# Optimization experiments

Hardware: AMD Instinct MI355X
Metric: run time of the kernel (lower is better)

The kernel has to match this reference:

```python
import jax, jax.numpy as jnp
from jax import lax
import numpy as np

BETA, TAU, NUM_ITER = 0.33, 1.0, 5
DN = ('NCDHW', 'OIDHW', 'NCDHW')


def _base_kernels():
    # 3x3x3 neighborhood-counting kernels from the torch module
    K_N6 = np.zeros((3, 3, 3), np.float32)
    for c in [(1, 1, 0), (1, 1, 2), (1, 0, 1), (1, 2, 1), (0, 1, 1), (2, 1, 1)]:
        K_N6[c] = 1.0
    K_N26 = np.ones((3, 3, 3), np.float32); K_N26[1, 1, 1] = 0.0
    K_N18 = K_N26.copy()
    for c in [(0, 0, 0), (0, 0, 2), (0, 2, 0), (0, 2, 2), (2, 0, 0), (2, 0, 2), (2, 2, 0), (2, 2, 2)]:
        K_N18[c] = 0.0
    K_B26 = np.zeros((3, 3, 3), np.float32)
    K_B26[0, 0, 0] = 1.0
    for c in [(0, 0, 1), (0, 1, 0), (0, 1, 1), (1, 0, 0), (1, 0, 1), (1, 1, 0)]:
        K_B26[c] = -1.0
    K_A6 = np.zeros((3, 3, 3), np.float32)
    K_A6[0, 1, 1] = -1.0
    for c in [(0, 0, 1), (0, 1, 0), (0, 1, 2), (0, 2, 1)]:
        K_A6[c] = 1.0
    return K_N6, K_N26, K_N18, K_B26, K_A6


def _stacked_weight():
    # Fuse all 17 simple-check convolutions into one conv over a 3-channel input
    # channel 0: img, channel 1: 1-img, channel 2: 2*img-1
    K_N6, K_N26, K_N18, K_B26, K_A6 = _base_kernels()
    b26 = [K_B26] + [np.flip(K_B26, ax) for ax in [(0,), (1,), (2,), (0, 1), (0, 2), (1, 2), (0, 1, 2)]]
    fA = np.flip(K_A6, 0)
    a6 = [K_A6, np.rot90(K_A6, axes=(0, 1)), np.rot90(K_A6, axes=(0, 2)),
          fA, np.rot90(fA, axes=(0, 1)), np.rot90(fA, axes=(0, 2))]
    rows = []
    def put(k, ch):
        w = np.zeros((3, 3, 3, 3), np.float32)
        w[ch] = k
        rows.append(w)
    put(K_N6, 1)   # counts bg 6-neighbors (applied to 1-img)
    put(K_N26, 0)  # counts fg 26-neighbors
    put(K_N18, 0)  # counts fg 18-neighbors
    for k in b26:
        put(k, 2)  # 8 B26-cell detectors on 2*img-1
    for k in a6:
        put(k, 2)  # 6 A6-cell detectors on 2*img-1
    return jnp.asarray(np.stack(rows)), jnp.asarray(K_N26).reshape(1, 1, 3, 3, 3)


W_SIMPLE, W_N26 = _stacked_weight()


def _clip01(x):  # F.hardtanh(x, 0, 1)
    return jnp.clip(x, 0.0, 1.0)


def _endpoint_check(img):
    p = jnp.pad(img, ((0, 0), (0, 0), (1, 1), (1, 1), (1, 1)))
    n26 = lax.conv_general_dilated(p, W_N26, (1, 1, 1), 'VALID', dimension_numbers=DN)
    return _clip01(2.0 - n26)  # endpoint iff <=1 fg 26-neighbor


def _simple_check(img):
    p = jnp.pad(img, ((0, 0), (0, 0), (1, 1), (1, 1), (1, 1)))
    x3 = jnp.concatenate([p, 1.0 - p, 2.0 * p - 1.0], axis=1)
    f = lax.conv_general_dilated(x3, W_SIMPLE, (2, 2, 2), 'VALID', dimension_numbers=DN)
    n6, n26, n18 = f[:, 0:1], f[:, 1:2], f[:, 2:3]
    num_b26 = jax.nn.relu(f[:, 3:11] - 6.0).sum(axis=1, keepdims=True)
    num_a6 = jax.nn.relu(f[:, 11:17] - 4.0).sum(axis=1, keepdims=True)
    cond1 = _clip01(n6) * _clip01(2.0 - n6)                              # exactly one bg 6-neighbor
    cond2 = _clip01(n26) * _clip01(2.0 - n26)                            # exactly one fg 26-neighbor
    cond3 = _clip01(n18) * _clip01(2.0 - n18) * _clip01(1.0 - num_b26)   # one 18-neighbor, no B26 cell
    cond4 = _clip01(n6 - 1.0) * _clip01(1.0 - num_a6) * _clip01(1.0 - num_b26)  # >=2 bg 6-nb, no A6/B26 cell
    return _clip01(cond1 + cond2 + cond3 + cond4)


def _forward(img):
    # _prepare_input: zero-pad each spatial dim by 1
    img = jnp.pad(img, ((0, 0), (0, 0), (1, 1), (1, 1), (1, 1)))
    # _stochastic_discretization (reparametrization + straight-through)
    alpha = (img + 1e-8) / (1.0 - img + 1e-8)
    u = jax.random.uniform(jax.random.key(42), img.shape, img.dtype, 1e-8, 1.0 - 1e-8)
    noise = jnp.log(u) - jnp.log1p(-u)
    soft = jax.nn.sigmoid((jnp.log(alpha) + noise * BETA) / TAU)
    img = lax.stop_gradient((soft > 0.5).astype(soft.dtype) - soft) + soft
    offsets = [(0, 0, 0), (1, 0, 0), (0, 1, 0), (1, 1, 0), (0, 0, 1), (1, 0, 1), (0, 1, 1), (1, 1, 1)]
    for _ in range(NUM_ITER):
        is_end = _endpoint_check(img)
        for xo, yo, zo in offsets:
            is_simple = _simple_check(img[:, :, xo:, yo:, zo:])
            sl = (slice(None), slice(None), slice(xo, None, 2), slice(yo, None, 2), slice(zo, None, 2))
            del_cand = is_simple * (1.0 - is_end[sl])
            img = img.at[sl].set(jnp.minimum(img[sl], 1.0 - del_cand))
    # _prepare_output: strip padding
    return img[:, :, 1:-1, 1:-1, 1:-1]


def setup_inputs():
    key = jax.random.key(0)
    img = jax.random.uniform(key, (2, 1, 160, 160, 160), jnp.float32)  # probabilities in [0,1)
    return {"img": img}


def reference(img):
    return _forward(img)
```

## Files before the change

### kernel.cpp

```cpp
#include <hip/hip_runtime.h>
#include <stdint.h>

#pragma clang fp contract(off)

#define PDIM 162
#define WPR  3
#define NW   (2*PDIM*PDIM*WPR)
#define OD   160
#define OD2  (160*160)
#define OD3  (160*160*160)
#define NOUT (2*OD3)
#define LSTR 4

__device__ __forceinline__ uint32_t rotl32(uint32_t x, uint32_t r) {
  return (x << r) | (x >> (32u - r));
}

__device__ __forceinline__ uint32_t threefry_bits(uint32_t idx) {
  const uint32_t ks0 = 0u, ks1 = 42u, ks2 = 0x1BD11BDAu ^ 0u ^ 42u;
  uint32_t x0 = 0u + ks0;
  uint32_t x1 = idx + ks1;
#define TFR(r) { x0 += x1; x1 = rotl32(x1, (r)); x1 ^= x0; }
  TFR(13u) TFR(15u) TFR(26u) TFR(6u)
  x0 += ks1; x1 += ks2 + 1u;
  TFR(17u) TFR(29u) TFR(16u) TFR(24u)
  x0 += ks2; x1 += ks0 + 2u;
  TFR(13u) TFR(15u) TFR(26u) TFR(6u)
  x0 += ks0; x1 += ks1 + 3u;
  TFR(17u) TFR(29u) TFR(16u) TFR(24u)
  x0 += ks1; x1 += ks2 + 4u;
  TFR(13u) TFR(15u) TFR(26u) TFR(6u)
  x0 += ks2; x1 += ks0 + 5u;
#undef TFR
  return x0 ^ x1;
}

__device__ __forceinline__ float xla_logf(float xin) {
  uint32_t bits = __float_as_uint(xin);
  float e = (float)((int)(bits >> 23) - 126);
  float x = __uint_as_float((bits & 0x007fffffu) | 0x3f000000u);
  const float SQRTHF = 0.707106781186547524f;
  bool lt = (x < SQRTHF);
  float tmp = lt ? x : 0.0f;
  e = e - (lt ? 1.0f : 0.0f);
  x = x - 1.0f;
  x = x + tmp;
  float z = x * x;
  float y = 7.0376836292e-2f;
  y = fmaf(y, x, -1.1514610310e-1f);
  y = fmaf(y, x,  1.1676998740e-1f);
  y = fmaf(y, x, -1.2420140846e-1f);
  y = fmaf(y, x,  1.4249322787e-1f);
  y = fmaf(y, x, -1.6668057665e-1f);
  y = fmaf(y, x,  2.0000714765e-1f);
  y = fmaf(y, x, -2.4999993993e-1f);
  y = fmaf(y, x,  3.3333331174e-1f);
  y = y * x;
  y = y * z;
  y = fmaf(e, -2.12194440e-4f, y);
  y = fmaf(-0.5f, z, y);
  x = x + y;
  x = fmaf(e, 0.693359375f, x);
  return x;
}

__device__ __forceinline__ float xla_log1pf(float x) {
  float for_large = xla_logf(x + 1.0f);
  float for_small = fmaf(-0.5f, x, 1.0f) * x;
  return (fabsf(x) < 1e-4f) ? for_small : for_large;
}

__global__ __launch_bounds__(256) void k_binarize(const float* __restrict__ in,
                                                  uint64_t* __restrict__ bits) {
  uint32_t t = blockIdx.x * 256u + threadIdx.x;
  uint32_t w = t >> 6, lane = t & 63u;
  if (w >= (uint32_t)NW) return;
  uint32_t row = w / 3u, wx = w - row * 3u;
  uint32_t n  = row / (uint32_t)(PDIM * PDIM);
  uint32_t rr = row - n * (uint32_t)(PDIM * PDIM);
  uint32_t z  = rr / (uint32_t)PDIM;
  uint32_t y  = rr - z * (uint32_t)PDIM;
  uint32_t x  = wx * 64u + lane;
  bool pred = false;
  if ((z - 1u) < 160u && (y - 1u) < 160u && (x - 1u) < 160u) {
    float v = in[((n * 160u + (z - 1u)) * 160u + (y - 1u)) * 160u + (x - 1u)];
    uint32_t i = row * 162u + x;
    uint32_t b = threefry_bits(i);
    float f  = __uint_as_float((b >> 9) | 0x3f800000u) - 1.0f;
    float uu = fmaxf(1e-8f, f + 1e-8f);
    float la = xla_logf((v + 1e-8f) / ((1.0f - v) + 1e-8f));
    float noise = xla_logf(uu) - xla_log1pf(-uu);
    float zs = la + noise * 0.33f;
    pred = (zs > 1.1920928955078125e-7f);
  }
  uint64_t m = __ballot(pred);
  if (lane == 0) bits[w] = m;
}

struct Nbhd { uint64_t V[3][3], Lb[3][3], Rb[3][3]; };

__device__ __forceinline__ void gather(const uint64_t* __restrict__ Bt,
                                       int lz, int ly, int w, Nbhd& N) {
#pragma unroll
  for (int dz = -1; dz <= 1; ++dz)
#pragma unroll
    for (int dy = -1; dy <= 1; ++dy) {
      const uint64_t* rp = &Bt[((lz + dz) * 32 + (ly + dy)) * LSTR];
      uint64_t r0 = rp[0], r1 = rp[1], r2 = rp[2];
      uint64_t b = (w == 0) ? r0 : ((w == 1) ? r1 : r2);
      uint64_t a = (w == 0) ? 0ull : ((w == 1) ? r0 : r1);
      uint64_t d = (w == 0) ? r1 : ((w == 1) ? r2 : 0ull);
      N.V [dz+1][dy+1] = b;
      N.Lb[dz+1][dy+1] = (b << 1) | (a >> 63);
      N.Rb[dz+1][dy+1] = (b >> 1) | (d << 63);
    }
}

#define NB(dz,dy,dx) ((dx)==-1 ? N.Lb[(dz)+1][(dy)+1] : ((dx)==1 ? N.Rb[(dz)+1][(dy)+1] : N.V[(dz)+1][(dy)+1]))

__global__ __launch_bounds__(1024) void k_iter(const uint64_t* __restrict__ bin,
                                               uint64_t* __restrict__ bout,
                                               int zero_pads) {
  __shared__ uint64_t Bt[32 * 32 * LSTR];
  __shared__ uint64_t Ge[32 * 32 * LSTR];
  const int tid = threadIdx.x;
  const int bid = blockIdx.x;
  const int n  = bid / 100;
  const int rm = bid - n * 100;
  const int tz = rm / 10, ty = rm - tz * 10;
  const int gz0 = 1 + 16 * tz, gy0 = 1 + 16 * ty;

  if (zero_pads && bid == 0) {
    for (int j = tid; j < 1288; j += 1024) {
      int nn, z, y;
      if (j < 648) { nn = j / 324; int r = j - nn * 324;
                     z = (r >= 162) ? 161 : 0; y = (r >= 162) ? r - 162 : r; }
      else { int j2 = j - 648; nn = j2 / 320; int r = j2 - nn * 320;
             y = (r >= 160) ? 161 : 0; z = 1 + ((r >= 160) ? r - 160 : r); }
      uint64_t* p = bout + (((nn * 162 + z) * 162) + y) * 3;
      p[0] = 0; p[1] = 0; p[2] = 0;
    }
  }

  for (int ti = tid; ti < 32 * 32 * 3; ti += 1024) {
    int lz = ti / 96, rem = ti - lz * 96, ly = rem / 3, w = rem - ly * 3;
    int z = gz0 - 8 + lz, y = gy0 - 8 + ly;
    uint64_t v = 0;
    if ((unsigned)z < 162u && (unsigned)y < 162u)
      v = bin[((n * 162 + z) * 162 + y) * 3 + w];
    Bt[(lz * 32 + ly) * LSTR + w] = v;
  }
  __syncthreads();

  for (int ti = tid; ti < 30 * 30 * 3; ti += 1024) {
    int q = ti / 90, rem = ti - q * 90;
    int lz = 1 + q, ly = 1 + rem / 3, w = rem - (rem / 3) * 3;
    uint64_t res = 0;
    if (Bt[(lz * 32 + ly) * LSTR + w] != 0ull) {
      Nbhd N; gather(Bt, lz, ly, w, N);
      uint64_t s = 0, c = 0;
#define ACC(bb) { uint64_t _b = (bb); c |= s & _b; s |= _b; }
#pragma unroll
      for (int dz = -1; dz <= 1; ++dz)
#pragma unroll
        for (int dy = -1; dy <= 1; ++dy) {
          ACC(NB(dz,dy,-1)); ACC(NB(dz,dy,1));
          if (dz != 0 || dy != 0) ACC(NB(dz,dy,0));
        }
#undef ACC
      res = c;
    }
    Ge[(lz * 32 + ly) * LSTR + w] = res;
  }
  __syncthreads();

  const int PLZ[8] = {1,0,1,0,1,0,1,0};
  const int PLY[8] = {1,1,0,0,1,1,0,0};
  for (int k = 0; k < 8; ++k) {
    const int h = 7 - k, cnt1 = 8 + h;
    const uint64_t xmask = (k < 4) ? 0x5555555555555555ull : 0xAAAAAAAAAAAAAAAAull;
    int s0 = 8 - h;
    const int slz = s0 + ((s0 ^ PLZ[k]) & 1);
    const int sly = s0 + ((s0 ^ PLY[k]) & 1);
    for (int ti = tid; ti < cnt1 * cnt1 * 3; ti += 1024) {
      int iz = ti / (cnt1 * 3), rem = ti - iz * (cnt1 * 3);
      int iy = rem / 3, w = rem - iy * 3;
      int lz = slz + 2 * iz, ly = sly + 2 * iy;
      uint64_t center = Bt[(lz * 32 + ly) * LSTR + w];
      uint64_t active = center & xmask & Ge[(lz * 32 + ly) * LSTR + w];
      if (active == 0ull) continue;
      Nbhd N; gather(Bt, lz, ly, w, N);

      uint64_t on = 0, tw = 0, fo = 0;
#define C6ADD(b) { uint64_t _u = on & (b); on ^= (b); uint64_t _v = tw & _u; tw ^= _u; fo |= _v; }
      C6ADD(NB(-1,0,0)) C6ADD(NB(1,0,0)) C6ADD(NB(0,-1,0))
      C6ADD(NB(0,1,0))  C6ADD(NB(0,0,-1)) C6ADD(NB(0,0,1))
#undef C6ADD
      uint64_t c6eq5 = fo & on & ~tw;
      uint64_t c6le4 = ~(fo & (on | tw));

      uint64_t s = 0, c2 = 0;
#define CS(b) { uint64_t _b = (b); c2 |= s & _b; s |= _b; }
      CS(NB(-1,0,0)) CS(NB(1,0,0)) CS(NB(0,-1,0)) CS(NB(0,1,0)) CS(NB(0,0,-1)) CS(NB(0,0,1))
      CS(NB(-1,-1,0)) CS(NB(-1,1,0)) CS(NB(-1,0,-1)) CS(NB(-1,0,1))
      CS(NB(1,-1,0))  CS(NB(1,1,0))  CS(NB(1,0,-1))  CS(NB(1,0,1))
      CS(NB(0,-1,-1)) CS(NB(0,-1,1)) CS(NB(0,1,-1))  CS(NB(0,1,1))
      uint64_t e18 = s & ~c2;
      CS(NB(-1,-1,-1)) CS(NB(-1,-1,1)) CS(NB(-1,1,-1)) CS(NB(-1,1,1))
      CS(NB(1,-1,-1))  CS(NB(1,-1,1))  CS(NB(1,1,-1))  CS(NB(1,1,1))
      uint64_t e26 = s & ~c2;
#undef CS

      uint64_t badB = 0;
#pragma unroll
      for (int sz = -1; sz <= 1; sz += 2)
#pragma unroll
        for (int sy = -1; sy <= 1; sy += 2)
#pragma unroll
          for (int sx = -1; sx <= 1; sx += 2) {
            uint64_t oct = NB(sz,0,0) | NB(0,sy,0) | NB(0,0,sx)
                         | NB(sz,sy,0) | NB(sz,0,sx) | NB(0,sy,sx);
            badB |= NB(sz,sy,sx) & ~oct;
          }
      uint64_t b0ok = ~badB;

      uint64_t badA = 0;
      badA |= ~NB(-1,0,0) & NB(-1,-1,0) & NB(-1,1,0) & NB(-1,0,-1) & NB(-1,0,1);
      badA |= ~NB( 1,0,0) & NB( 1,-1,0) & NB( 1,1,0) & NB( 1,0,-1) & NB( 1,0,1);
      badA |= ~NB(0,-1,0) & NB(-1,-1,0) & NB(1,-1,0) & NB(0,-1,-1) & NB(0,-1,1);
      badA |= ~NB(0, 1,0) & NB(-1, 1,0) & NB(1, 1,0) & NB(0, 1,-1) & NB(0, 1,1);
      badA |= ~NB(0,0,-1) & NB(-1,0,-1) & NB(1,0,-1) & NB(0,-1,-1) & NB(0,1,-1);
      badA |= ~NB(0,0, 1) & NB(-1,0, 1) & NB(1,0, 1) & NB(0,-1, 1) & NB(0,1, 1);
      uint64_t a0ok = ~badA;

      uint64_t simple = c6eq5 | e26 | (e18 & b0ok) | (c6le4 & a0ok & b0ok);
      uint64_t del = simple & active;
      if (del) Bt[(lz * 32 + ly) * LSTR + w] = center & ~del;
    }
    __syncthreads();
  }

  for (int ti = tid; ti < 16 * 16 * 3; ti += 1024) {
    int iz = ti / 48, rem = ti - iz * 48, iy = rem / 3, w = rem - iy * 3;
    bout[((n * 162 + gz0 + iz) * 162 + (gy0 + iy)) * 3 + w] =
        Bt[((8 + iz) * 32 + (8 + iy)) * LSTR + w];
  }
}

__global__ __launch_bounds__(256) void k_output(const uint64_t* __restrict__ bits,
                                                float4* __restrict__ out) {
  uint32_t t = blockIdx.x * 256u + threadIdx.x;
  if (t >= (uint32_t)(NOUT / 4)) return;
  uint32_t i = t * 4u;
  uint32_t n = i / (uint32_t)OD3;
  uint32_t r = i - n * (uint32_t)OD3;
  uint32_t z = r / (uint32_t)OD2; r -= z * (uint32_t)OD2;
  uint32_t y = r / (uint32_t)OD;
  uint32_t x = r - y * (uint32_t)OD;
  uint32_t row = (n * 162u + z + 1u) * 162u + (y + 1u);
  uint32_t bi = x + 1u;
  uint32_t wx = bi >> 6, sft = bi & 63u;
  uint64_t v = bits[row * 3u + wx] >> sft;
  if (sft > 60u) v |= bits[row * 3u + wx + 1u] << (64u - sft);
  out[t] = make_float4((float)(v & 1u), (float)((v >> 1) & 1u),
                       (float)((v >> 2) & 1u), (float)((v >> 3) & 1u));
}

extern "C" void kernel_launch(void* const* d_in, const int* in_sizes, int n_in,
                              void* d_out, int out_size, void* d_ws, size_t ws_size,
                              hipStream_t stream) {
  const float* in = (const float*)d_in[0];
  float4* out = (float4*)d_out;
  uint64_t* A = (uint64_t*)d_ws;
  uint64_t* B = A + NW;

  k_binarize<<<dim3((NW * 64 + 255) / 256), dim3(256), 0, stream>>>(in, A);
  k_iter<<<dim3(200), dim3(1024), 0, stream>>>(A, B, 1);
  k_iter<<<dim3(200), dim3(1024), 0, stream>>>(B, A, 0);
  k_iter<<<dim3(200), dim3(1024), 0, stream>>>(A, B, 0);
  k_iter<<<dim3(200), dim3(1024), 0, stream>>>(B, A, 0);
  k_iter<<<dim3(200), dim3(1024), 0, stream>>>(A, B, 0);
  k_output<<<dim3((NOUT / 4 + 255) / 256), dim3(256), 0, stream>>>(B, out);
}
```

Before: 236.4 us.

## Process all three words of a row per thread and shrink block to 512

Each thread now loads the 3x3 neighbourhood rows once and evaluates all three 64-bit words of a row, instead of one thread per word, each re-reading the shared rows. The shared tile layout drops the padded stride of 4 for a packed stride (105 words per z-plane), and the block size falls from 1024 to 512 threads. The aim is fewer redundant LDS reads and less index arithmetic. The cost is higher register pressure and fewer parallel work items per sweep, so later sweeps with small counts may leave threads idle.

```diff
diff --git a/kernel.cpp b/kernel.cpp
--- a/kernel.cpp
+++ b/kernel.cpp
@@ -4,13 +4,14 @@
 #pragma clang fp contract(off)
 
 #define PDIM 162
-#define WPR  3
-#define NW   (2*PDIM*PDIM*WPR)
+#define NW   (2*PDIM*PDIM*3)
 #define OD   160
 #define OD2  (160*160)
 #define OD3  (160*160*160)
 #define NOUT (2*OD3)
-#define LSTR 4
+#define PZ   105
+#define LIDX(lz,ly) ((lz)*PZ + (ly)*3)
+#define BTHR 512
 
 __device__ __forceinline__ uint32_t rotl32(uint32_t x, uint32_t r) {
   return (x << r) | (x >> (32u - r));
@@ -97,32 +98,26 @@
   if (lane == 0) bits[w] = m;
 }
 
-struct Nbhd { uint64_t V[3][3], Lb[3][3], Rb[3][3]; };
-
-__device__ __forceinline__ void gather(const uint64_t* __restrict__ Bt,
-                                       int lz, int ly, int w, Nbhd& N) {
-#pragma unroll
-  for (int dz = -1; dz <= 1; ++dz)
-#pragma unroll
-    for (int dy = -1; dy <= 1; ++dy) {
-      const uint64_t* rp = &Bt[((lz + dz) * 32 + (ly + dy)) * LSTR];
-      uint64_t r0 = rp[0], r1 = rp[1], r2 = rp[2];
-      uint64_t b = (w == 0) ? r0 : ((w == 1) ? r1 : r2);
-      uint64_t a = (w == 0) ? 0ull : ((w == 1) ? r0 : r1);
-      uint64_t d = (w == 0) ? r1 : ((w == 1) ? r2 : 0ull);
-      N.V [dz+1][dy+1] = b;
-      N.Lb[dz+1][dy+1] = (b << 1) | (a >> 63);
-      N.Rb[dz+1][dy+1] = (b >> 1) | (d << 63);
+#define NB(dz,dy,dx) ((dx)==-1 ? Lb[(dz)+1][(dy)+1] : ((dx)==1 ? Rb[(dz)+1][(dy)+1] : Vv[(dz)+1][(dy)+1]))
+
+#define EXPAND_W(w_) \
+  _Pragma("unroll") \
+  for (int dz = 0; dz < 3; ++dz) \
+    _Pragma("unroll") \
+    for (int dy = 0; dy < 3; ++dy) { \
+      uint64_t b = R[dz][dy][w_]; \
+      uint64_t a = ((w_) > 0) ? R[dz][dy][(w_)-1] : 0ull; \
+      uint64_t d = ((w_) < 2) ? R[dz][dy][(w_)+1] : 0ull; \
+      Vv[dz][dy] = b; \
+      Lb[dz][dy] = (b << 1) | (a >> 63); \
+      Rb[dz][dy] = (b >> 1) | (d << 63); \
     }
-}
-
-#define NB(dz,dy,dx) ((dx)==-1 ? N.Lb[(dz)+1][(dy)+1] : ((dx)==1 ? N.Rb[(dz)+1][(dy)+1] : N.V[(dz)+1][(dy)+1]))
-
-__global__ __launch_bounds__(1024) void k_iter(const uint64_t* __restrict__ bin,
+
+__global__ __launch_bounds__(BTHR) void k_iter(const uint64_t* __restrict__ bin,
                                                uint64_t* __restrict__ bout,
                                                int zero_pads) {
-  __shared__ uint64_t Bt[32 * 32 * LSTR];
-  __shared__ uint64_t Ge[32 * 32 * LSTR];
+  __shared__ uint64_t Bt[32 * PZ];
+  __shared__ uint64_t Ge[32 * PZ];
   const int tid = threadIdx.x;
   const int bid = blockIdx.x;
   const int n  = bid / 100;
@@ -131,7 +126,7 @@
   const int gz0 = 1 + 16 * tz, gy0 = 1 + 16 * ty;
 
   if (zero_pads && bid == 0) {
-    for (int j = tid; j < 1288; j += 1024) {
+    for (int j = tid; j < 1288; j += BTHR) {
       int nn, z, y;
       if (j < 648) { nn = j / 324; int r = j - nn * 324;
                      z = (r >= 162) ? 161 : 0; y = (r >= 162) ? r - 162 : r; }
@@ -142,22 +137,35 @@
     }
   }
 
-  for (int ti = tid; ti < 32 * 32 * 3; ti += 1024) {
+  for (int ti = tid; ti < 32 * 32 * 3; ti += BTHR) {
     int lz = ti / 96, rem = ti - lz * 96, ly = rem / 3, w = rem - ly * 3;
     int z = gz0 - 8 + lz, y = gy0 - 8 + ly;
     uint64_t v = 0;
     if ((unsigned)z < 162u && (unsigned)y < 162u)
       v = bin[((n * 162 + z) * 162 + y) * 3 + w];
-    Bt[(lz * 32 + ly) * LSTR + w] = v;
+    Bt[LIDX(lz, ly) + w] = v;
   }
   __syncthreads();
 
-  for (int ti = tid; ti < 30 * 30 * 3; ti += 1024) {
-    int q = ti / 90, rem = ti - q * 90;
-    int lz = 1 + q, ly = 1 + rem / 3, w = rem - (rem / 3) * 3;
-    uint64_t res = 0;
-    if (Bt[(lz * 32 + ly) * LSTR + w] != 0ull) {
-      Nbhd N; gather(Bt, lz, ly, w, N);
+  for (int ti = tid; ti < 30 * 30; ti += BTHR) {
+    int iz = ti % 30, iy = ti / 30;
+    int lz = 1 + iz, ly = 1 + iy;
+    int base = LIDX(lz, ly);
+    uint64_t c0 = Bt[base], c1 = Bt[base + 1], c2w = Bt[base + 2];
+    if ((c0 | c1 | c2w) == 0ull) { Ge[base] = 0; Ge[base+1] = 0; Ge[base+2] = 0; continue; }
+    uint64_t R[3][3][3];
+#pragma unroll
+    for (int dz = 0; dz < 3; ++dz)
+#pragma unroll
+      for (int dy = 0; dy < 3; ++dy) {
+        int rb = LIDX(lz + dz - 1, ly + dy - 1);
+        R[dz][dy][0] = Bt[rb]; R[dz][dy][1] = Bt[rb + 1]; R[dz][dy][2] = Bt[rb + 2];
+      }
+    uint64_t res[3];
+#pragma unroll
+    for (int w = 0; w < 3; ++w) {
+      uint64_t Vv[3][3], Lb[3][3], Rb[3][3];
+      EXPAND_W(w)
       uint64_t s = 0, c = 0;
 #define ACC(bb) { uint64_t _b = (bb); c |= s & _b; s |= _b; }
 #pragma unroll
@@ -168,9 +176,9 @@
           if (dz != 0 || dy != 0) ACC(NB(dz,dy,0));
         }
 #undef ACC
-      res = c;
+      res[w] = c;
     }
-    Ge[(lz * 32 + ly) * LSTR + w] = res;
+    Ge[base] = res[0]; Ge[base + 1] = res[1]; Ge[base + 2] = res[2];
   }
   __syncthreads();
 
@@ -182,68 +190,85 @@
     int s0 = 8 - h;
     const int slz = s0 + ((s0 ^ PLZ[k]) & 1);
     const int sly = s0 + ((s0 ^ PLY[k]) & 1);
-    for (int ti = tid; ti < cnt1 * cnt1 * 3; ti += 1024) {
-      int iz = ti / (cnt1 * 3), rem = ti - iz * (cnt1 * 3);
-      int iy = rem / 3, w = rem - iy * 3;
+    for (int ti = tid; ti < cnt1 * cnt1; ti += BTHR) {
+      int iz = ti % cnt1, iy = ti / cnt1;
       int lz = slz + 2 * iz, ly = sly + 2 * iy;
-      uint64_t center = Bt[(lz * 32 + ly) * LSTR + w];
-      uint64_t active = center & xmask & Ge[(lz * 32 + ly) * LSTR + w];
-      if (active == 0ull) continue;
-      Nbhd N; gather(Bt, lz, ly, w, N);
-
-      uint64_t on = 0, tw = 0, fo = 0;
+      int base = LIDX(lz, ly);
+      uint64_t center[3], active[3];
+#pragma unroll
+      for (int w = 0; w < 3; ++w) {
+        center[w] = Bt[base + w];
+        active[w] = center[w] & xmask & Ge[base + w];
+      }
+      if ((active[0] | active[1] | active[2]) == 0ull) continue;
+      uint64_t R[3][3][3];
+#pragma unroll
+      for (int dz = 0; dz < 3; ++dz)
+#pragma unroll
+        for (int dy = 0; dy < 3; ++dy) {
+          int rb = LIDX(lz + dz - 1, ly + dy - 1);
+          R[dz][dy][0] = Bt[rb]; R[dz][dy][1] = Bt[rb + 1]; R[dz][dy][2] = Bt[rb + 2];
+        }
+#pragma unroll
+      for (int w = 0; w < 3; ++w) {
+        if (active[w] == 0ull) continue;
+        uint64_t Vv[3][3], Lb[3][3], Rb[3][3];
+        EXPAND_W(w)
+
+        uint64_t on = 0, tw = 0, fo = 0;
 #define C6ADD(b) { uint64_t _u = on & (b); on ^= (b); uint64_t _v = tw & _u; tw ^= _u; fo |= _v; }
-      C6ADD(NB(-1,0,0)) C6ADD(NB(1,0,0)) C6ADD(NB(0,-1,0))
-      C6ADD(NB(0,1,0))  C6ADD(NB(0,0,-1)) C6ADD(NB(0,0,1))
+        C6ADD(NB(-1,0,0)) C6ADD(NB(1,0,0)) C6ADD(NB(0,-1,0))
+        C6ADD(NB(0,1,0))  C6ADD(NB(0,0,-1)) C6ADD(NB(0,0,1))
 #undef C6ADD
-      uint64_t c6eq5 = fo & on & ~tw;
-      uint64_t c6le4 = ~(fo & (on | tw));
-
-      uint64_t s = 0, c2 = 0;
+        uint64_t c6eq5 = fo & on & ~tw;
+        uint64_t c6le4 = ~(fo & (on | tw));
+
+        uint64_t s = 0, c2 = 0;
 #define CS(b) { uint64_t _b = (b); c2 |= s & _b; s |= _b; }
-      CS(NB(-1,0,0)) CS(NB(1,0,0)) CS(NB(0,-1,0)) CS(NB(0,1,0)) CS(NB(0,0,-1)) CS(NB(0,0,1))
-      CS(NB(-1,-1,0)) CS(NB(-1,1,0)) CS(NB(-1,0,-1)) CS(NB(-1,0,1))
-      CS(NB(1,-1,0))  CS(NB(1,1,0))  CS(NB(1,0,-1))  CS(NB(1,0,1))
-      CS(NB(0,-1,-1)) CS(NB(0,-1,1)) CS(NB(0,1,-1))  CS(NB(0,1,1))
-      uint64_t e18 = s & ~c2;
-      CS(NB(-1,-1,-1)) CS(NB(-1,-1,1)) CS(NB(-1,1,-1)) CS(NB(-1,1,1))
-      CS(NB(1,-1,-1))  CS(NB(1,-1,1))  CS(NB(1,1,-1))  CS(NB(1,1,1))
-      uint64_t e26 = s & ~c2;
+        CS(NB(-1,0,0)) CS(NB(1,0,0)) CS(NB(0,-1,0)) CS(NB(0,1,0)) CS(NB(0,0,-1)) CS(NB(0,0,1))
+        CS(NB(-1,-1,0)) CS(NB(-1,1,0)) CS(NB(-1,0,-1)) CS(NB(-1,0,1))
+        CS(NB(1,-1,0))  CS(NB(1,1,0))  CS(NB(1,0,-1))  CS(NB(1,0,1))
+        CS(NB(0,-1,-1)) CS(NB(0,-1,1)) CS(NB(0,1,-1))  CS(NB(0,1,1))
+        uint64_t e18 = s & ~c2;
+        CS(NB(-1,-1,-1)) CS(NB(-1,-1,1)) CS(NB(-1,1,-1)) CS(NB(-1,1,1))
+        CS(NB(1,-1,-1))  CS(NB(1,-1,1))  CS(NB(1,1,-1))  CS(NB(1,1,1))
+        uint64_t e26 = s & ~c2;
 #undef CS
 
-      uint64_t badB = 0;
-#pragma unroll
-      for (int sz = -1; sz <= 1; sz += 2)
-#pragma unroll
-        for (int sy = -1; sy <= 1; sy += 2)
-#pragma unroll
-          for (int sx = -1; sx <= 1; sx += 2) {
-            uint64_t oct = NB(sz,0,0) | NB(0,sy,0) | NB(0,0,sx)
-                         | NB(sz,sy,0) | NB(sz,0,sx) | NB(0,sy,sx);
-            badB |= NB(sz,sy,sx) & ~oct;
-          }
-      uint64_t b0ok = ~badB;
-
-      uint64_t badA = 0;
-      badA |= ~NB(-1,0,0) & NB(-1,-1,0) & NB(-1,1,0) & NB(-1,0,-1) & NB(-1,0,1);
-      badA |= ~NB( 1,0,0) & NB( 1,-1,0) & NB( 1,1,0) & NB( 1,0,-1) & NB( 1,0,1);
-      badA |= ~NB(0,-1,0) & NB(-1,-1,0) & NB(1,-1,0) & NB(0,-1,-1) & NB(0,-1,1);
-      badA |= ~NB(0, 1,0) & NB(-1, 1,0) & NB(1, 1,0) & NB(0, 1,-1) & NB(0, 1,1);
-      badA |= ~NB(0,0,-1) & NB(-1,0,-1) & NB(1,0,-1) & NB(0,-1,-1) & NB(0,1,-1);
-      badA |= ~NB(0,0, 1) & NB(-1,0, 1) & NB(1,0, 1) & NB(0,-1, 1) & NB(0,1, 1);
-      uint64_t a0ok = ~badA;
-
-      uint64_t simple = c6eq5 | e26 | (e18 & b0ok) | (c6le4 & a0ok & b0ok);
-      uint64_t del = simple & active;
-      if (del) Bt[(lz * 32 + ly) * LSTR + w] = center & ~del;
+        uint64_t badB = 0;
+#pragma unroll
+        for (int sz = -1; sz <= 1; sz += 2)
+#pragma unroll
+          for (int sy = -1; sy <= 1; sy += 2)
+#pragma unroll
+            for (int sx = -1; sx <= 1; sx += 2) {
+              uint64_t oct = NB(sz,0,0) | NB(0,sy,0) | NB(0,0,sx)
+                           | NB(sz,sy,0) | NB(sz,0,sx) | NB(0,sy,sx);
+              badB |= NB(sz,sy,sx) & ~oct;
+            }
+        uint64_t b0ok = ~badB;
+
+        uint64_t badA = 0;
+        badA |= ~NB(-1,0,0) & NB(-1,-1,0) & NB(-1,1,0) & NB(-1,0,-1) & NB(-1,0,1);
+        badA |= ~NB( 1,0,0) & NB( 1,-1,0) & NB( 1,1,0) & NB( 1,0,-1) & NB( 1,0,1);
+        badA |= ~NB(0,-1,0) & NB(-1,-1,0) & NB(1,-1,0) & NB(0,-1,-1) & NB(0,-1,1);
+        badA |= ~NB(0, 1,0) & NB(-1, 1,0) & NB(1, 1,0) & NB(0, 1,-1) & NB(0, 1,1);
+        badA |= ~NB(0,0,-1) & NB(-1,0,-1) & NB(1,0,-1) & NB(0,-1,-1) & NB(0,1,-1);
+        badA |= ~NB(0,0, 1) & NB(-1,0, 1) & NB(1,0, 1) & NB(0,-1, 1) & NB(0,1, 1);
+        uint64_t a0ok = ~badA;
+
+        uint64_t simple = c6eq5 | e26 | (e18 & b0ok) | (c6le4 & a0ok & b0ok);
+        uint64_t del = simple & active[w];
+        if (del) Bt[base + w] = center[w] & ~del;
+      }
     }
     __syncthreads();
   }
 
-  for (int ti = tid; ti < 16 * 16 * 3; ti += 1024) {
+  for (int ti = tid; ti < 16 * 16 * 3; ti += BTHR) {
     int iz = ti / 48, rem = ti - iz * 48, iy = rem / 3, w = rem - iy * 3;
     bout[((n * 162 + gz0 + iz) * 162 + (gy0 + iy)) * 3 + w] =
-        Bt[((8 + iz) * 32 + (8 + iy)) * LSTR + w];
+        Bt[LIDX(8 + iz, 8 + iy) + w];
   }
 }
 
@@ -275,10 +300,10 @@
   uint64_t* B = A + NW;
 
   k_binarize<<<dim3((NW * 64 + 255) / 256), dim3(256), 0, stream>>>(in, A);
-  k_iter<<<dim3(200), dim3(1024), 0, stream>>>(A, B, 1);
-  k_iter<<<dim3(200), dim3(1024), 0, stream>>>(B, A, 0);
-  k_iter<<<dim3(200), dim3(1024), 0, stream>>>(A, B, 0);
-  k_iter<<<dim3(200), dim3(1024), 0, stream>>>(B, A, 0);
-  k_iter<<<dim3(200), dim3(1024), 0, stream>>>(A, B, 0);
+  k_iter<<<dim3(200), dim3(BTHR), 0, stream>>>(A, B, 1);
+  k_iter<<<dim3(200), dim3(BTHR), 0, stream>>>(B, A, 0);
+  k_iter<<<dim3(200), dim3(BTHR), 0, stream>>>(A, B, 0);
+  k_iter<<<dim3(200), dim3(BTHR), 0, stream>>>(B, A, 0);
+  k_iter<<<dim3(200), dim3(BTHR), 0, stream>>>(A, B, 0);
   k_output<<<dim3((NOUT / 4 + 255) / 256), dim3(256), 0, stream>>>(B, out);
 }
```

After: 254.8 us. +7.8%, slower.

## Shrink iteration tiles to 8x8 with 256-thread blocks and bank-skewed LDS layout

Applied to the files above, without the earlier changes.

Each iteration kernel now owns an 8x8 (z,y) output tile with an 8-row halo (24x24 loaded) instead of a 16x16 tile, and launches 800 blocks of 256 threads instead of 200 blocks of 1024. Shared memory uses a new layout with z-parity interleaving and a row pitch of 73 words, meant to reduce bank conflicts and drop the padding. The aim is better occupancy and more blocks across the CUs. The cost is much more redundant halo work: the loaded area per output grows from 4x to 9x, and the per-subiteration loops are small.

```diff
diff --git a/kernel.cpp b/kernel.cpp
--- a/kernel.cpp
+++ b/kernel.cpp
@@ -4,13 +4,15 @@
 #pragma clang fp contract(off)
 
 #define PDIM 162
-#define WPR  3
-#define NW   (2*PDIM*PDIM*WPR)
+#define NW   (2*PDIM*PDIM*3)
 #define OD   160
 #define OD2  (160*160)
 #define OD3  (160*160*160)
 #define NOUT (2*OD3)
-#define LSTR 4
+
+#define PY 73
+#define LZI(lz) ((((lz) & 1) * 12) + ((lz) >> 1))
+#define LADDR(lz,ly) (LZI(lz) * PY + (ly) * 3)
 
 __device__ __forceinline__ uint32_t rotl32(uint32_t x, uint32_t r) {
   return (x << r) | (x >> (32u - r));
@@ -97,41 +99,37 @@
   if (lane == 0) bits[w] = m;
 }
 
-struct Nbhd { uint64_t V[3][3], Lb[3][3], Rb[3][3]; };
-
-__device__ __forceinline__ void gather(const uint64_t* __restrict__ Bt,
-                                       int lz, int ly, int w, Nbhd& N) {
-#pragma unroll
-  for (int dz = -1; dz <= 1; ++dz)
-#pragma unroll
-    for (int dy = -1; dy <= 1; ++dy) {
-      const uint64_t* rp = &Bt[((lz + dz) * 32 + (ly + dy)) * LSTR];
-      uint64_t r0 = rp[0], r1 = rp[1], r2 = rp[2];
-      uint64_t b = (w == 0) ? r0 : ((w == 1) ? r1 : r2);
-      uint64_t a = (w == 0) ? 0ull : ((w == 1) ? r0 : r1);
-      uint64_t d = (w == 0) ? r1 : ((w == 1) ? r2 : 0ull);
-      N.V [dz+1][dy+1] = b;
-      N.Lb[dz+1][dy+1] = (b << 1) | (a >> 63);
-      N.Rb[dz+1][dy+1] = (b >> 1) | (d << 63);
-    }
-}
-
-#define NB(dz,dy,dx) ((dx)==-1 ? N.Lb[(dz)+1][(dy)+1] : ((dx)==1 ? N.Rb[(dz)+1][(dy)+1] : N.V[(dz)+1][(dy)+1]))
-
-__global__ __launch_bounds__(1024) void k_iter(const uint64_t* __restrict__ bin,
-                                               uint64_t* __restrict__ bout,
-                                               int zero_pads) {
-  __shared__ uint64_t Bt[32 * 32 * LSTR];
-  __shared__ uint64_t Ge[32 * 32 * LSTR];
+#define NB(dz,dy,dx) ((dx)==-1 ? Lb[(dz)+1][(dy)+1] : ((dx)==1 ? Rb[(dz)+1][(dy)+1] : Vv[(dz)+1][(dy)+1]))
+
+#define GATHER_W(SRC, lz, ly, w) \
+  _Pragma("unroll") \
+  for (int dz = 0; dz < 3; ++dz) \
+    _Pragma("unroll") \
+    for (int dy = 0; dy < 3; ++dy) { \
+      int rb = LADDR((lz) + dz - 1, (ly) + dy - 1); \
+      uint64_t r0 = SRC[rb], r1 = SRC[rb + 1], r2 = SRC[rb + 2]; \
+      uint64_t b = ((w) == 0) ? r0 : (((w) == 1) ? r1 : r2); \
+      uint64_t a = ((w) == 0) ? 0ull : (((w) == 1) ? r0 : r1); \
+      uint64_t d = ((w) == 0) ? r1 : (((w) == 1) ? r2 : 0ull); \
+      Vv[dz][dy] = b; \
+      Lb[dz][dy] = (b << 1) | (a >> 63); \
+      Rb[dz][dy] = (b >> 1) | (d << 63); \
+    }
+
+__global__ __launch_bounds__(256) void k_iter(const uint64_t* __restrict__ bin,
+                                              uint64_t* __restrict__ bout,
+                                              int zero_pads) {
+  __shared__ uint64_t Bt[1752];
+  __shared__ uint64_t Ge[1752];
   const int tid = threadIdx.x;
   const int bid = blockIdx.x;
-  const int n  = bid / 100;
-  const int rm = bid - n * 100;
-  const int tz = rm / 10, ty = rm - tz * 10;
-  const int gz0 = 1 + 16 * tz, gy0 = 1 + 16 * ty;
+  const int n  = bid / 400;
+  const int rm = bid - n * 400;
+  const int tz = rm / 20, ty = rm - tz * 20;
+  const int gz0 = 1 + 8 * tz, gy0 = 1 + 8 * ty;
 
   if (zero_pads && bid == 0) {
-    for (int j = tid; j < 1288; j += 1024) {
+    for (int j = tid; j < 1288; j += 256) {
       int nn, z, y;
       if (j < 648) { nn = j / 324; int r = j - nn * 324;
                      z = (r >= 162) ? 161 : 0; y = (r >= 162) ? r - 162 : r; }
@@ -142,22 +140,24 @@
     }
   }
 
-  for (int ti = tid; ti < 32 * 32 * 3; ti += 1024) {
-    int lz = ti / 96, rem = ti - lz * 96, ly = rem / 3, w = rem - ly * 3;
+  for (int ti = tid; ti < 24 * 24 * 3; ti += 256) {
+    int w = ti % 3, r = ti / 3, ly = r % 24, lz = r / 24;
     int z = gz0 - 8 + lz, y = gy0 - 8 + ly;
     uint64_t v = 0;
     if ((unsigned)z < 162u && (unsigned)y < 162u)
       v = bin[((n * 162 + z) * 162 + y) * 3 + w];
-    Bt[(lz * 32 + ly) * LSTR + w] = v;
+    Bt[LADDR(lz, ly) + w] = v;
   }
   __syncthreads();
 
-  for (int ti = tid; ti < 30 * 30 * 3; ti += 1024) {
-    int q = ti / 90, rem = ti - q * 90;
-    int lz = 1 + q, ly = 1 + rem / 3, w = rem - (rem / 3) * 3;
+  for (int ti = tid; ti < 22 * 22 * 3; ti += 256) {
+    int w = ti % 3, r = ti / 3, iz = r % 22, iy = r / 22;
+    int lz = 1 + iz, ly = 1 + iy;
+    int base = LADDR(lz, ly) + w;
     uint64_t res = 0;
-    if (Bt[(lz * 32 + ly) * LSTR + w] != 0ull) {
-      Nbhd N; gather(Bt, lz, ly, w, N);
+    if (Bt[base] != 0ull) {
+      uint64_t Vv[3][3], Lb[3][3], Rb[3][3];
+      GATHER_W(Bt, lz, ly, w)
       uint64_t s = 0, c = 0;
 #define ACC(bb) { uint64_t _b = (bb); c |= s & _b; s |= _b; }
 #pragma unroll
@@ -170,26 +170,27 @@
 #undef ACC
       res = c;
     }
-    Ge[(lz * 32 + ly) * LSTR + w] = res;
+    Ge[base] = res;
   }
   __syncthreads();
 
   const int PLZ[8] = {1,0,1,0,1,0,1,0};
   const int PLY[8] = {1,1,0,0,1,1,0,0};
   for (int k = 0; k < 8; ++k) {
-    const int h = 7 - k, cnt1 = 8 + h;
+    const int h = 7 - k, cnt = 4 + h;
     const uint64_t xmask = (k < 4) ? 0x5555555555555555ull : 0xAAAAAAAAAAAAAAAAull;
     int s0 = 8 - h;
     const int slz = s0 + ((s0 ^ PLZ[k]) & 1);
     const int sly = s0 + ((s0 ^ PLY[k]) & 1);
-    for (int ti = tid; ti < cnt1 * cnt1 * 3; ti += 1024) {
-      int iz = ti / (cnt1 * 3), rem = ti - iz * (cnt1 * 3);
-      int iy = rem / 3, w = rem - iy * 3;
+    for (int ti = tid; ti < cnt * cnt * 3; ti += 256) {
+      int w = ti % 3, r = ti / 3, iz = r % cnt, iy = r / cnt;
       int lz = slz + 2 * iz, ly = sly + 2 * iy;
-      uint64_t center = Bt[(lz * 32 + ly) * LSTR + w];
-      uint64_t active = center & xmask & Ge[(lz * 32 + ly) * LSTR + w];
+      int base = LADDR(lz, ly) + w;
+      uint64_t center = Bt[base];
+      uint64_t active = center & xmask & Ge[base];
       if (active == 0ull) continue;
-      Nbhd N; gather(Bt, lz, ly, w, N);
+      uint64_t Vv[3][3], Lb[3][3], Rb[3][3];
+      GATHER_W(Bt, lz, ly, w)
 
       uint64_t on = 0, tw = 0, fo = 0;
 #define C6ADD(b) { uint64_t _u = on & (b); on ^= (b); uint64_t _v = tw & _u; tw ^= _u; fo |= _v; }
@@ -235,15 +236,15 @@
 
       uint64_t simple = c6eq5 | e26 | (e18 & b0ok) | (c6le4 & a0ok & b0ok);
       uint64_t del = simple & active;
-      if (del) Bt[(lz * 32 + ly) * LSTR + w] = center & ~del;
+      if (del) Bt[base] = center & ~del;
     }
     __syncthreads();
   }
 
-  for (int ti = tid; ti < 16 * 16 * 3; ti += 1024) {
-    int iz = ti / 48, rem = ti - iz * 48, iy = rem / 3, w = rem - iy * 3;
+  for (int ti = tid; ti < 8 * 8 * 3; ti += 256) {
+    int w = ti % 3, r = ti / 3, iy = r % 8, iz = r / 8;
     bout[((n * 162 + gz0 + iz) * 162 + (gy0 + iy)) * 3 + w] =
-        Bt[((8 + iz) * 32 + (8 + iy)) * LSTR + w];
+        Bt[LADDR(8 + iz, 8 + iy) + w];
   }
 }
 
@@ -275,10 +276,10 @@
   uint64_t* B = A + NW;
 
   k_binarize<<<dim3((NW * 64 + 255) / 256), dim3(256), 0, stream>>>(in, A);
-  k_iter<<<dim3(200), dim3(1024), 0, stream>>>(A, B, 1);
-  k_iter<<<dim3(200), dim3(1024), 0, stream>>>(B, A, 0);
-  k_iter<<<dim3(200), dim3(1024), 0, stream>>>(A, B, 0);
-  k_iter<<<dim3(200), dim3(1024), 0, stream>>>(B, A, 0);
-  k_iter<<<dim3(200), dim3(1024), 0, stream>>>(A, B, 0);
+  k_iter<<<dim3(800), dim3(256), 0, stream>>>(A, B, 1);
+  k_iter<<<dim3(800), dim3(256), 0, stream>>>(B, A, 0);
+  k_iter<<<dim3(800), dim3(256), 0, stream>>>(A, B, 0);
+  k_iter<<<dim3(800), dim3(256), 0, stream>>>(B, A, 0);
+  k_iter<<<dim3(800), dim3(256), 0, stream>>>(A, B, 0);
   k_output<<<dim3((NOUT / 4 + 255) / 256), dim3(256), 0, stream>>>(B, out);
 }
```

New measurement: 345.7 us. 1.46x slower.
